# Optimization experiments

Measured on AMD Instinct MI355X. Metric: run time of the kernel, lower is better.

## Reference

```python
import jax, jax.numpy as jnp
import numpy as np

N, L, H, D = 4, 2048, 16, 32   # batch, seq len, heads, projection_dim
DIM = H * D                     # 512 model dim


def setup_inputs() -> dict:
    rng = jax.random.key(0)
    k1, k2, k3, k4, k5 = jax.random.split(rng, 5)
    query = jax.random.normal(k1, (N, L, DIM), dtype=jnp.float32)
    key = jax.random.normal(k2, (N, L, DIM), dtype=jnp.float32)
    scale = 0.02
    Wq = jax.random.normal(k3, (DIM, DIM), dtype=jnp.float32) * scale
    Wk = jax.random.normal(k4, (DIM, DIM), dtype=jnp.float32) * scale
    Wv = jax.random.normal(k5, (DIM, DIM), dtype=jnp.float32) * scale
    return {"query": query, "key": key, "Wq": Wq, "Wk": Wk, "Wv": Wv, "mask": 1}


def reference(query, key, Wq, Wk, Wv, mask):
    # torch Linear(bias=False): y = x @ W^T
    n, Lq, _ = query.shape
    _, Lk, _ = key.shape
    q = (query @ Wq.T).reshape(n, Lq, H, D).transpose(0, 2, 1, 3)  # (N,H,Lq,D)
    k = (key @ Wk.T).reshape(n, Lk, H, D).transpose(0, 2, 1, 3)    # (N,H,Lk,D)
    v = (key @ Wv.T).reshape(n, Lk, H, D).transpose(0, 2, 1, 3)    # (N,H,Lk,D)
    q = jax.nn.softmax(q, axis=-1)
    k = jax.nn.softmax(k, axis=-1)
    # causal branch (mask truthy): Lq*Lk > D^2*Lk, so the module takes the
    # cumsum-of-outer-products ("right") path:
    #   right = cumsum_l( k_l outer v_l );  out_l = q_l @ right_l
    kv = jnp.einsum('nhld,nhle->nhlde', k, v)   # (N,H,Lk,D,D) outer products
    S = jnp.cumsum(kv, axis=2)                  # running prefix state
    out = jnp.einsum('nhld,nhlde->nhle', q, S)  # (N,H,Lq,D)
    return out.transpose(0, 2, 1, 3).reshape(n, Lq, H * D)
```

## Files before the change

kernel.cpp:

```cpp
#include <hip/hip_runtime.h>

#define NB      4
#define L_SEQ   2048
#define H_HEADS 16
#define D32     32
#define DIM     512
#define NH      (NB * H_HEADS)
#define CHUNK   64
#define NCHUNK  (L_SEQ / CHUNK)

typedef __attribute__((ext_vector_type(8))) short bf16x8;
typedef __attribute__((ext_vector_type(4))) float f32x4;

__device__ __forceinline__ unsigned short f2bf(float x) {
    unsigned u = __float_as_uint(x);
    u += 0x7fff + ((u >> 16) & 1);
    return (unsigned short)(u >> 16);
}
__device__ __forceinline__ unsigned pack2(float lo, float hi) {
    return (unsigned)f2bf(lo) | ((unsigned)f2bf(hi) << 16);
}

#define QN  4194304
#define WN  262144
#define TOT (2*QN + 3*WN)
__global__ __launch_bounds__(256) void convert_kernel(
    const float* __restrict__ query, const float* __restrict__ key,
    const float* __restrict__ Wq, const float* __restrict__ Wk,
    const float* __restrict__ Wv, unsigned short* __restrict__ dst)
{
    int idx = (blockIdx.x * 256 + threadIdx.x) * 8;
    const float* src; int off;
    if (idx < QN)               { src = query; off = idx; }
    else if (idx < 2*QN)        { src = key;   off = idx - QN; }
    else if (idx < 2*QN + WN)   { src = Wq;    off = idx - 2*QN; }
    else if (idx < 2*QN + 2*WN) { src = Wk;    off = idx - 2*QN - WN; }
    else                        { src = Wv;    off = idx - 2*QN - 2*WN; }
    float4 a = *(const float4*)(src + off);
    float4 b = *(const float4*)(src + off + 4);
    *(uint4*)(dst + idx) = make_uint4(pack2(a.x, a.y), pack2(a.z, a.w),
                                      pack2(b.x, b.y), pack2(b.z, b.w));
}

__global__ __launch_bounds__(256) void gemm3_mfma_kernel(
    const unsigned short* __restrict__ qb, const unsigned short* __restrict__ kb2,
    const unsigned short* __restrict__ wqb, const unsigned short* __restrict__ wkb,
    const unsigned short* __restrict__ wvb,
    unsigned short* __restrict__ Qs, unsigned short* __restrict__ Ks,
    unsigned short* __restrict__ Vt)
{
    const int z  = blockIdx.z;
    const int bx = blockIdx.x >> 6;
    const int by = blockIdx.x & 63;
    const unsigned short *PA, *PB;
    int m0, n0;
    if (z == 0)      { PA = qb;  PB = wqb; m0 = by*128; n0 = bx*128; }
    else if (z == 1) { PA = kb2; PB = wkb; m0 = by*128; n0 = bx*128; }
    else             { PA = wvb; PB = kb2; m0 = bx*128; n0 = by*128; }

    __shared__ unsigned short Asm[128 * 32];
    __shared__ unsigned short Bsm[128 * 32];

    const int t    = threadIdx.x;
    const int w    = t >> 6;
    const int lane = t & 63;
    const int wm   = w >> 1, wn = w & 1;
    const int chunkoff = ((lane & 15) * 4 + (lane >> 4)) * 8;

    f32x4 acc[4][4] = {};

    for (int kb = 0; kb < DIM; kb += 32) {
        #pragma unroll
        for (int rep = 0; rep < 2; rep++) {
            int li  = t + rep * 256;
            int row = li >> 2, kq = li & 3;
            uint4 av = *(const uint4*)(PA + (size_t)(m0 + row) * DIM + kb + kq * 8);
            uint4 bv = *(const uint4*)(PB + (size_t)(n0 + row) * DIM + kb + kq * 8);
            ((uint4*)Asm)[li] = av;
            ((uint4*)Bsm)[li] = bv;
        }
        __syncthreads();

        bf16x8 af[4], bfr[4];
        #pragma unroll
        for (int i = 0; i < 4; i++)
            af[i] = *(const bf16x8*)(Asm + (wm * 4 + i) * 512 + chunkoff);
        #pragma unroll
        for (int j = 0; j < 4; j++)
            bfr[j] = *(const bf16x8*)(Bsm + (wn * 4 + j) * 512 + chunkoff);
        #pragma unroll
        for (int i = 0; i < 4; i++)
            #pragma unroll
            for (int j = 0; j < 4; j++)
                acc[i][j] = __builtin_amdgcn_mfma_f32_16x16x32_bf16(
                    af[i], bfr[j], acc[i][j], 0, 0, 0);
        __syncthreads();
    }

    if (z < 2) {
        #pragma unroll
        for (int i = 0; i < 4; i++)
            #pragma unroll
            for (int jp = 0; jp < 2; jp++)
                #pragma unroll
                for (int r = 0; r < 4; r++) {
                    float a = acc[i][2 * jp][r], b = acc[i][2 * jp + 1][r];
                    float m = fmaxf(a, b);
                    #pragma unroll
                    for (int off = 1; off < 16; off <<= 1)
                        m = fmaxf(m, __shfl_xor(m, off, 64));
                    float ea = __expf(a - m), eb = __expf(b - m);
                    float s = ea + eb;
                    #pragma unroll
                    for (int off = 1; off < 16; off <<= 1)
                        s += __shfl_xor(s, off, 64);
                    float inv = 1.0f / s;
                    acc[i][2 * jp][r]     = ea * inv;
                    acc[i][2 * jp + 1][r] = eb * inv;
                }
    }

    const int quad = lane >> 4, lm = lane & 15;
    #pragma unroll
    for (int i = 0; i < 4; i++) {
        int rbase = m0 + wm * 64 + i * 16 + quad * 4;
        #pragma unroll
        for (int r = 0; r < 4; r++) {
            int rg = rbase + r;
            #pragma unroll
            for (int j = 0; j < 4; j++) {
                int cg = n0 + wn * 64 + j * 16 + lm;
                unsigned short val = f2bf(acc[i][j][r]);
                if (z < 2) {
                    int n = rg >> 11, l = rg & 2047;
                    int h = cg >> 5,  e = cg & 31;
                    unsigned short* dp = (z == 0) ? Qs : Ks;
                    dp[(((size_t)(n * H_HEADS + h)) * L_SEQ + l) * D32 + e] = val;
                } else {
                    int h = rg >> 5,  e = rg & 31;
                    int n = cg >> 11, l = cg & 2047;
                    Vt[(((size_t)(n * H_HEADS + h)) * D32 + e) * L_SEQ + l] = val;
                }
            }
        }
    }
}

__global__ __launch_bounds__(64) void chunk_kv_mfma_kernel(
    const unsigned short* __restrict__ Ks, const unsigned short* __restrict__ Vt,
    float* __restrict__ ckvT)
{
    const int c = blockIdx.x, nh = blockIdx.y;
    const int lane = threadIdx.x;
    const int lm = lane & 15, quad = lane >> 4;

    __shared__ unsigned short Kl[64 * 36];

    {
        const unsigned short* kg = Ks + ((size_t)nh * L_SEQ + c * CHUNK + lane) * D32;
        #pragma unroll
        for (int i = 0; i < 4; i++) {
            uint4 v = *(const uint4*)(kg + i * 8);
            *(uint4*)(Kl + lane * 36 + i * 8) = v;
        }
    }
    __syncthreads();

    f32x4 acc[2][2] = {};
    #pragma unroll
    for (int ch = 0; ch < 2; ch++) {
        bf16x8 aV[2], bK[2];
        #pragma unroll
        for (int mt = 0; mt < 2; mt++)
            aV[mt] = *(const bf16x8*)(Vt + ((size_t)nh * D32 + mt * 16 + lm) * L_SEQ
                                         + c * CHUNK + ch * 32 + quad * 8);
        #pragma unroll
        for (int nt = 0; nt < 2; nt++) {
            const unsigned short* kp = Kl + (ch * 32 + quad * 8) * 36 + nt * 16 + lm;
            #pragma unroll
            for (int j = 0; j < 8; j++) bK[nt][j] = (short)kp[j * 36];
        }
        #pragma unroll
        for (int mt = 0; mt < 2; mt++)
            #pragma unroll
            for (int nt = 0; nt < 2; nt++)
                acc[mt][nt] = __builtin_amdgcn_mfma_f32_16x16x32_bf16(
                    aV[mt], bK[nt], acc[mt][nt], 0, 0, 0);
    }
    #pragma unroll
    for (int mt = 0; mt < 2; mt++)
        #pragma unroll
        for (int nt = 0; nt < 2; nt++)
            #pragma unroll
            for (int r = 0; r < 4; r++) {
                int e = mt * 16 + quad * 4 + r;
                int d = nt * 16 + lm;
                ckvT[(((size_t)nh * NCHUNK + c) * 32 + e) * 32 + d] = acc[mt][nt][r];
            }
}

__global__ __launch_bounds__(64) void prefix_kernel(
    const float* __restrict__ ckvT, unsigned short* __restrict__ SpT)
{
    int nh   = blockIdx.y;
    int slot = blockIdx.x * 64 + threadIdx.x;
    const float* base = ckvT + (size_t)nh * NCHUNK * 1024 + slot * 4;
    unsigned short* sp = SpT + (size_t)nh * NCHUNK * 1024 + slot * 4;
    float4 acc = make_float4(0.f, 0.f, 0.f, 0.f);
    #pragma unroll
    for (int cb = 0; cb < NCHUNK; cb += 8) {
        float4 v[8];
        #pragma unroll
        for (int j = 0; j < 8; j++)
            v[j] = *(const float4*)(base + (size_t)(cb + j) * 1024);
        #pragma unroll
        for (int j = 0; j < 8; j++) {
            ushort4 u;
            u.x = f2bf(acc.x); u.y = f2bf(acc.y);
            u.z = f2bf(acc.z); u.w = f2bf(acc.w);
            *(ushort4*)(sp + (size_t)(cb + j) * 1024) = u;
            acc.x += v[j].x; acc.y += v[j].y;
            acc.z += v[j].z; acc.w += v[j].w;
        }
    }
}

__global__ __launch_bounds__(64) void chunk_out_mfma_kernel(
    const unsigned short* __restrict__ Qs, const unsigned short* __restrict__ Ks,
    const unsigned short* __restrict__ Vt, const unsigned short* __restrict__ SpT,
    float* __restrict__ out)
{
    const int c = blockIdx.x, nh = blockIdx.y;
    __shared__ unsigned short P[64 * 72];

    const int lane = threadIdx.x;
    const int lm = lane & 15, quad = lane >> 4;

    bf16x8 aQ[4], bK[4];
    #pragma unroll
    for (int i = 0; i < 4; i++)
        aQ[i] = *(const bf16x8*)(Qs + ((size_t)nh * L_SEQ + c * CHUNK + i * 16 + lm) * D32
                                    + quad * 8);
    #pragma unroll
    for (int j = 0; j < 4; j++)
        bK[j] = *(const bf16x8*)(Ks + ((size_t)nh * L_SEQ + c * CHUNK + j * 16 + lm) * D32
                                    + quad * 8);

    #pragma unroll
    for (int i = 0; i < 4; i++) {
        #pragma unroll
        for (int j = 0; j < 4; j++) {
            f32x4 p = {};
            if (j <= i) {
                p = __builtin_amdgcn_mfma_f32_16x16x32_bf16(aQ[i], bK[j], p, 0, 0, 0);
                if (j == i) {
                    #pragma unroll
                    for (int r = 0; r < 4; r++)
                        if (lm > quad * 4 + r) p[r] = 0.f;
                }
            }
            #pragma unroll
            for (int r = 0; r < 4; r++)
                P[(i * 16 + quad * 4 + r) * 72 + j * 16 + lm] = f2bf(p[r]);
        }
    }
    __syncthreads();

    bf16x8 bS[2], bV[2][2];
    #pragma unroll
    for (int nt = 0; nt < 2; nt++) {
        bS[nt] = *(const bf16x8*)(SpT + (((size_t)nh * NCHUNK + c) * 32 + nt * 16 + lm) * 32
                                      + quad * 8);
        #pragma unroll
        for (int ch = 0; ch < 2; ch++)
            bV[nt][ch] = *(const bf16x8*)(Vt + ((size_t)nh * D32 + nt * 16 + lm) * L_SEQ
                                             + c * CHUNK + ch * 32 + quad * 8);
    }

    const int n = nh >> 4, h = nh & 15;
    #pragma unroll
    for (int i = 0; i < 4; i++) {
        const int chmax = (i >> 1) + 1;
        bf16x8 aP[2];
        for (int ch = 0; ch < chmax; ch++)
            aP[ch] = *(const bf16x8*)&P[(i * 16 + lm) * 72 + ch * 32 + quad * 8];
        #pragma unroll
        for (int nt = 0; nt < 2; nt++) {
            f32x4 acc = {};
            acc = __builtin_amdgcn_mfma_f32_16x16x32_bf16(aQ[i], bS[nt], acc, 0, 0, 0);
            for (int ch = 0; ch < chmax; ch++)
                acc = __builtin_amdgcn_mfma_f32_16x16x32_bf16(aP[ch], bV[nt][ch], acc, 0, 0, 0);
            #pragma unroll
            for (int r = 0; r < 4; r++) {
                int lg = c * CHUNK + i * 16 + quad * 4 + r;
                out[((size_t)n * L_SEQ + lg) * DIM + h * D32 + nt * 16 + lm] = acc[r];
            }
        }
    }
}

extern "C" void kernel_launch(void* const* d_in, const int* in_sizes, int n_in,
                              void* d_out, int out_size, void* d_ws, size_t ws_size,
                              hipStream_t stream)
{
    (void)in_sizes; (void)n_in; (void)out_size; (void)ws_size;
    const float* query = (const float*)d_in[0];
    const float* key   = (const float*)d_in[1];
    const float* Wq    = (const float*)d_in[2];
    const float* Wk    = (const float*)d_in[3];
    const float* Wv    = (const float*)d_in[4];
    float* out = (float*)d_out;

    unsigned short* bf = (unsigned short*)d_ws;
    unsigned short* qb  = bf;
    unsigned short* kb  = qb + QN;
    unsigned short* wqb = kb + QN;
    unsigned short* wkb = wqb + WN;
    unsigned short* wvb = wkb + WN;
    unsigned short* Qs  = wvb + WN;
    const size_t SZ = (size_t)NH * L_SEQ * D32;
    unsigned short* Ks  = Qs + SZ;
    unsigned short* Vt  = Ks + SZ;
    unsigned short* SpT = Vt + SZ;
    float* ckvT = (float*)(SpT + (size_t)NH * NCHUNK * 1024);

    convert_kernel<<<dim3(TOT / (256 * 8)), dim3(256), 0, stream>>>(
        query, key, Wq, Wk, Wv, qb);
    gemm3_mfma_kernel<<<dim3(256, 1, 3), dim3(256), 0, stream>>>(
        qb, kb, wqb, wkb, wvb, Qs, Ks, Vt);
    chunk_kv_mfma_kernel<<<dim3(NCHUNK, NH), dim3(64), 0, stream>>>(Ks, Vt, ckvT);
    prefix_kernel<<<dim3(4, NH), dim3(64), 0, stream>>>(ckvT, SpT);
    chunk_out_mfma_kernel<<<dim3(NCHUNK, NH), dim3(64), 0, stream>>>(Qs, Ks, Vt, SpT, out);
}
```

Baseline: 140.8 us.

## Pad GEMM LDS tiles and process two chunks per block in chunk kernels

The projection GEMM's shared-memory A/B tiles are padded from 32 to 40 elements per row so that MFMA fragment reads hit fewer bank conflicts. The chunk_kv and chunk_out kernels now each handle two consecutive chunks per 64-thread block, which halves the grid size and amortizes per-block launch and setup overhead. The cost is more LDS and registers per block and fewer blocks available to hide latency.

New measurement: 141.7 us. About the same (+0.6%).

```diff
diff --git a/kernel.cpp b/kernel.cpp
--- a/kernel.cpp
+++ b/kernel.cpp
@@ -58,14 +58,14 @@
     else if (z == 1) { PA = kb2; PB = wkb; m0 = by*128; n0 = bx*128; }
     else             { PA = wvb; PB = kb2; m0 = bx*128; n0 = by*128; }
 
-    __shared__ unsigned short Asm[128 * 32];
-    __shared__ unsigned short Bsm[128 * 32];
+    __shared__ unsigned short Asm[128 * 40];
+    __shared__ unsigned short Bsm[128 * 40];
 
     const int t    = threadIdx.x;
     const int w    = t >> 6;
     const int lane = t & 63;
     const int wm   = w >> 1, wn = w & 1;
-    const int chunkoff = ((lane & 15) * 4 + (lane >> 4)) * 8;
+    const int chunkoff = (lane & 15) * 40 + (lane >> 4) * 8;
 
     f32x4 acc[4][4] = {};
 
@@ -76,18 +76,18 @@
             int row = li >> 2, kq = li & 3;
             uint4 av = *(const uint4*)(PA + (size_t)(m0 + row) * DIM + kb + kq * 8);
             uint4 bv = *(const uint4*)(PB + (size_t)(n0 + row) * DIM + kb + kq * 8);
-            ((uint4*)Asm)[li] = av;
-            ((uint4*)Bsm)[li] = bv;
+            ((uint4*)Asm)[row * 5 + kq] = av;
+            ((uint4*)Bsm)[row * 5 + kq] = bv;
         }
         __syncthreads();
 
         bf16x8 af[4], bfr[4];
         #pragma unroll
         for (int i = 0; i < 4; i++)
-            af[i] = *(const bf16x8*)(Asm + (wm * 4 + i) * 512 + chunkoff);
+            af[i] = *(const bf16x8*)(Asm + (wm * 4 + i) * 640 + chunkoff);
         #pragma unroll
         for (int j = 0; j < 4; j++)
-            bfr[j] = *(const bf16x8*)(Bsm + (wn * 4 + j) * 512 + chunkoff);
+            bfr[j] = *(const bf16x8*)(Bsm + (wn * 4 + j) * 640 + chunkoff);
         #pragma unroll
         for (int i = 0; i < 4; i++)
             #pragma unroll
@@ -150,53 +150,60 @@
     const unsigned short* __restrict__ Ks, const unsigned short* __restrict__ Vt,
     float* __restrict__ ckvT)
 {
-    const int c = blockIdx.x, nh = blockIdx.y;
+    const int c0 = blockIdx.x * 2, nh = blockIdx.y;
     const int lane = threadIdx.x;
     const int lm = lane & 15, quad = lane >> 4;
 
-    __shared__ unsigned short Kl[64 * 36];
-
-    {
-        const unsigned short* kg = Ks + ((size_t)nh * L_SEQ + c * CHUNK + lane) * D32;
+    __shared__ unsigned short Kl[2][64 * 36];
+
+    #pragma unroll
+    for (int cc = 0; cc < 2; cc++) {
+        const unsigned short* kg = Ks + ((size_t)nh * L_SEQ + (c0 + cc) * CHUNK + lane) * D32;
         #pragma unroll
         for (int i = 0; i < 4; i++) {
             uint4 v = *(const uint4*)(kg + i * 8);
-            *(uint4*)(Kl + lane * 36 + i * 8) = v;
+            *(uint4*)(&Kl[cc][lane * 36 + i * 8]) = v;
         }
     }
     __syncthreads();
 
-    f32x4 acc[2][2] = {};
-    #pragma unroll
-    for (int ch = 0; ch < 2; ch++) {
-        bf16x8 aV[2], bK[2];
+    f32x4 acc[2][2][2] = {};
+    #pragma unroll
+    for (int cc = 0; cc < 2; cc++) {
+        #pragma unroll
+        for (int ch = 0; ch < 2; ch++) {
+            bf16x8 aV[2], bK[2];
+            #pragma unroll
+            for (int mt = 0; mt < 2; mt++)
+                aV[mt] = *(const bf16x8*)(Vt + ((size_t)nh * D32 + mt * 16 + lm) * L_SEQ
+                                             + (c0 + cc) * CHUNK + ch * 32 + quad * 8);
+            #pragma unroll
+            for (int nt = 0; nt < 2; nt++) {
+                const unsigned short* kp = &Kl[cc][(ch * 32 + quad * 8) * 36 + nt * 16 + lm];
+                #pragma unroll
+                for (int j = 0; j < 8; j++) bK[nt][j] = (short)kp[j * 36];
+            }
+            #pragma unroll
+            for (int mt = 0; mt < 2; mt++)
+                #pragma unroll
+                for (int nt = 0; nt < 2; nt++)
+                    acc[cc][mt][nt] = __builtin_amdgcn_mfma_f32_16x16x32_bf16(
+                        aV[mt], bK[nt], acc[cc][mt][nt], 0, 0, 0);
+        }
+    }
+    #pragma unroll
+    for (int cc = 0; cc < 2; cc++)
         #pragma unroll
         for (int mt = 0; mt < 2; mt++)
-            aV[mt] = *(const bf16x8*)(Vt + ((size_t)nh * D32 + mt * 16 + lm) * L_SEQ
-                                         + c * CHUNK + ch * 32 + quad * 8);
-        #pragma unroll
-        for (int nt = 0; nt < 2; nt++) {
-            const unsigned short* kp = Kl + (ch * 32 + quad * 8) * 36 + nt * 16 + lm;
-            #pragma unroll
-            for (int j = 0; j < 8; j++) bK[nt][j] = (short)kp[j * 36];
-        }
-        #pragma unroll
-        for (int mt = 0; mt < 2; mt++)
             #pragma unroll
             for (int nt = 0; nt < 2; nt++)
-                acc[mt][nt] = __builtin_amdgcn_mfma_f32_16x16x32_bf16(
-                    aV[mt], bK[nt], acc[mt][nt], 0, 0, 0);
-    }
-    #pragma unroll
-    for (int mt = 0; mt < 2; mt++)
-        #pragma unroll
-        for (int nt = 0; nt < 2; nt++)
-            #pragma unroll
-            for (int r = 0; r < 4; r++) {
-                int e = mt * 16 + quad * 4 + r;
-                int d = nt * 16 + lm;
-                ckvT[(((size_t)nh * NCHUNK + c) * 32 + e) * 32 + d] = acc[mt][nt][r];
-            }
+                #pragma unroll
+                for (int r = 0; r < 4; r++) {
+                    int e = mt * 16 + quad * 4 + r;
+                    int d = nt * 16 + lm;
+                    ckvT[(((size_t)nh * NCHUNK + c0 + cc) * 32 + e) * 32 + d] =
+                        acc[cc][mt][nt][r];
+                }
 }
 
 __global__ __launch_bounds__(64) void prefix_kernel(
@@ -230,70 +237,78 @@
     const unsigned short* __restrict__ Vt, const unsigned short* __restrict__ SpT,
     float* __restrict__ out)
 {
-    const int c = blockIdx.x, nh = blockIdx.y;
-    __shared__ unsigned short P[64 * 72];
+    const int c0 = blockIdx.x * 2, nh = blockIdx.y;
+    __shared__ unsigned short P[2][64 * 72];
 
     const int lane = threadIdx.x;
     const int lm = lane & 15, quad = lane >> 4;
 
-    bf16x8 aQ[4], bK[4];
-    #pragma unroll
-    for (int i = 0; i < 4; i++)
-        aQ[i] = *(const bf16x8*)(Qs + ((size_t)nh * L_SEQ + c * CHUNK + i * 16 + lm) * D32
-                                    + quad * 8);
-    #pragma unroll
-    for (int j = 0; j < 4; j++)
-        bK[j] = *(const bf16x8*)(Ks + ((size_t)nh * L_SEQ + c * CHUNK + j * 16 + lm) * D32
-                                    + quad * 8);
-
-    #pragma unroll
-    for (int i = 0; i < 4; i++) {
-        #pragma unroll
-        for (int j = 0; j < 4; j++) {
-            f32x4 p = {};
-            if (j <= i) {
-                p = __builtin_amdgcn_mfma_f32_16x16x32_bf16(aQ[i], bK[j], p, 0, 0, 0);
-                if (j == i) {
-                    #pragma unroll
-                    for (int r = 0; r < 4; r++)
-                        if (lm > quad * 4 + r) p[r] = 0.f;
-                }
+    bf16x8 aQ[2][4];
+    #pragma unroll
+    for (int cc = 0; cc < 2; cc++)
+        #pragma unroll
+        for (int i = 0; i < 4; i++)
+            aQ[cc][i] = *(const bf16x8*)(Qs + ((size_t)nh * L_SEQ + (c0 + cc) * CHUNK
+                                               + i * 16 + lm) * D32 + quad * 8);
+
+    #pragma unroll
+    for (int cc = 0; cc < 2; cc++) {
+        bf16x8 bK[4];
+        #pragma unroll
+        for (int j = 0; j < 4; j++)
+            bK[j] = *(const bf16x8*)(Ks + ((size_t)nh * L_SEQ + (c0 + cc) * CHUNK
+                                           + j * 16 + lm) * D32 + quad * 8);
+        #pragma unroll
+        for (int i = 0; i < 4; i++) {
+            #pragma unroll
+            for (int j = 0; j < 4; j++) {
+                f32x4 p = {};
+                if (j <= i) {
+                    p = __builtin_amdgcn_mfma_f32_16x16x32_bf16(aQ[cc][i], bK[j], p, 0, 0, 0);
+                    if (j == i) {
+                        #pragma unroll
+                        for (int r = 0; r < 4; r++)
+                            if (lm > quad * 4 + r) p[r] = 0.f;
+                    }
+                }
+                #pragma unroll
+                for (int r = 0; r < 4; r++)
+                    P[cc][(i * 16 + quad * 4 + r) * 72 + j * 16 + lm] = f2bf(p[r]);
             }
-            #pragma unroll
-            for (int r = 0; r < 4; r++)
-                P[(i * 16 + quad * 4 + r) * 72 + j * 16 + lm] = f2bf(p[r]);
         }
     }
     __syncthreads();
 
-    bf16x8 bS[2], bV[2][2];
-    #pragma unroll
-    for (int nt = 0; nt < 2; nt++) {
-        bS[nt] = *(const bf16x8*)(SpT + (((size_t)nh * NCHUNK + c) * 32 + nt * 16 + lm) * 32
-                                      + quad * 8);
-        #pragma unroll
-        for (int ch = 0; ch < 2; ch++)
-            bV[nt][ch] = *(const bf16x8*)(Vt + ((size_t)nh * D32 + nt * 16 + lm) * L_SEQ
-                                             + c * CHUNK + ch * 32 + quad * 8);
-    }
-
     const int n = nh >> 4, h = nh & 15;
     #pragma unroll
-    for (int i = 0; i < 4; i++) {
-        const int chmax = (i >> 1) + 1;
-        bf16x8 aP[2];
-        for (int ch = 0; ch < chmax; ch++)
-            aP[ch] = *(const bf16x8*)&P[(i * 16 + lm) * 72 + ch * 32 + quad * 8];
+    for (int cc = 0; cc < 2; cc++) {
+        bf16x8 bS[2], bV[2][2];
         #pragma unroll
         for (int nt = 0; nt < 2; nt++) {
-            f32x4 acc = {};
-            acc = __builtin_amdgcn_mfma_f32_16x16x32_bf16(aQ[i], bS[nt], acc, 0, 0, 0);
+            bS[nt] = *(const bf16x8*)(SpT + (((size_t)nh * NCHUNK + c0 + cc) * 32
+                                             + nt * 16 + lm) * 32 + quad * 8);
+            #pragma unroll
+            for (int ch = 0; ch < 2; ch++)
+                bV[nt][ch] = *(const bf16x8*)(Vt + ((size_t)nh * D32 + nt * 16 + lm) * L_SEQ
+                                                 + (c0 + cc) * CHUNK + ch * 32 + quad * 8);
+        }
+        #pragma unroll
+        for (int i = 0; i < 4; i++) {
+            const int chmax = (i >> 1) + 1;
+            bf16x8 aP[2];
             for (int ch = 0; ch < chmax; ch++)
-                acc = __builtin_amdgcn_mfma_f32_16x16x32_bf16(aP[ch], bV[nt][ch], acc, 0, 0, 0);
-            #pragma unroll
-            for (int r = 0; r < 4; r++) {
-                int lg = c * CHUNK + i * 16 + quad * 4 + r;
-                out[((size_t)n * L_SEQ + lg) * DIM + h * D32 + nt * 16 + lm] = acc[r];
+                aP[ch] = *(const bf16x8*)&P[cc][(i * 16 + lm) * 72 + ch * 32 + quad * 8];
+            #pragma unroll
+            for (int nt = 0; nt < 2; nt++) {
+                f32x4 acc = {};
+                acc = __builtin_amdgcn_mfma_f32_16x16x32_bf16(aQ[cc][i], bS[nt], acc, 0, 0, 0);
+                for (int ch = 0; ch < chmax; ch++)
+                    acc = __builtin_amdgcn_mfma_f32_16x16x32_bf16(aP[ch], bV[nt][ch], acc, 0, 0, 0);
+                #pragma unroll
+                for (int r = 0; r < 4; r++) {
+                    int lg = (c0 + cc) * CHUNK + i * 16 + quad * 4 + r;
+                    out[((size_t)n * L_SEQ + lg) * DIM + h * D32 + nt * 16 + lm] = acc[r];
+                }
             }
         }
     }
@@ -328,7 +343,7 @@
         query, key, Wq, Wk, Wv, qb);
     gemm3_mfma_kernel<<<dim3(256, 1, 3), dim3(256), 0, stream>>>(
         qb, kb, wqb, wkb, wvb, Qs, Ks, Vt);
-    chunk_kv_mfma_kernel<<<dim3(NCHUNK, NH), dim3(64), 0, stream>>>(Ks, Vt, ckvT);
+    chunk_kv_mfma_kernel<<<dim3(NCHUNK / 2, NH), dim3(64), 0, stream>>>(Ks, Vt, ckvT);
     prefix_kernel<<<dim3(4, NH), dim3(64), 0, stream>>>(ckvT, SpT);
-    chunk_out_mfma_kernel<<<dim3(NCHUNK, NH), dim3(64), 0, stream>>>(Qs, Ks, Vt, SpT, out);
-}
+    chunk_out_mfma_kernel<<<dim3(NCHUNK / 2, NH), dim3(64), 0, stream>>>(Qs, Ks, Vt, SpT, out);
+}
```
